# Performance work log

Hardware: AMD Instinct MI355X
Metric: run time of the kernel (lower is better)

## Reference

```python
import jax, jax.numpy as jnp
import numpy as np

N, D, C = 262144, 128, 64  # flattened tokens, feat_dim, num_classes (subjects)


def setup_inputs() -> dict:
    key = jax.random.key(0)
    k1, k2, k3 = jax.random.split(key, 3)
    feature = jax.random.normal(k1, (N, D), dtype=jnp.float32)
    label = jax.random.randint(k2, (N,), 0, C, dtype=jnp.int64)
    centers = jax.random.normal(k3, (C, D), dtype=jnp.float32)  # nn.Parameter torch.randn
    return {"feature": feature, "label": label, "centers": centers}


def reference(feature, label, centers):
    f = feature.reshape(-1, feature.shape[1])            # [N, D]
    lbl = label.reshape(-1)                              # [N]
    num_classes = centers.shape[0]

    # Pairwise squared distances ||f_i - c_j||^2, via expansion to avoid the
    # [N, C, D] broadcast intermediate the torch code materializes.
    f2 = jnp.sum(f * f, axis=1, keepdims=True)           # [N, 1]
    c2 = jnp.sum(centers * centers, axis=1)              # [C]
    distance_centers = f2 + c2[None, :] - 2.0 * (f @ centers.T)  # [N, C]

    centers_batch = centers[lbl]                         # [N, D] gather
    center_loss = jnp.mean((f - centers_batch) ** 2)     # MSELoss (mean reduction)

    diff = centers_batch - f                             # [N, D]
    # segment-reduce replacing the per-unique-label python loop
    sums = jax.ops.segment_sum(diff, lbl, num_segments=num_classes)      # [C, D]
    counts = jnp.bincount(lbl, length=num_classes)                        # [C]
    difference = sums / jnp.clip(counts, 1, None).astype(f.dtype)[:, None]

    return (center_loss, difference, distance_centers)
```

## Files before the change

kernel.cpp:

```cpp
#include <hip/hip_runtime.h>
#include <hip/hip_bf16.h>

#define N_TOK 262144
#define D_FEAT 128
#define C_CLS 64
#define TILE_M 128
#define DIST_BLOCKS 1024
#define BLOCK_T 256
#define TILES_PER_BLOCK 2
#define NSTEP (TILES_PER_BLOCK * 2)
#define SEG_ELEMS (C_CLS * D_FEAT)
#define SEG_BLOCKS 1024
#define SEG_ROWS_B (N_TOK / SEG_BLOCKS)
#define SEG_KSTEPS (SEG_ROWS_B / 32)

typedef __attribute__((ext_vector_type(8))) short bf16x8;
typedef __attribute__((ext_vector_type(4))) float f32x4;

__device__ __forceinline__ short f2bf(float x) {
    return (short)__bfloat16_as_ushort(__float2bfloat16(x));
}

__device__ __forceinline__ bf16x8 pack8(float4 a, float4 b) {
    bf16x8 t;
    t[0] = f2bf(a.x); t[1] = f2bf(a.y); t[2] = f2bf(a.z); t[3] = f2bf(a.w);
    t[4] = f2bf(b.x); t[5] = f2bf(b.y); t[6] = f2bf(b.z); t[7] = f2bf(b.w);
    return t;
}

__device__ __forceinline__ void gload_lds16(const float* g, float* l) {
    __builtin_amdgcn_global_load_lds(
        (const __attribute__((address_space(1))) void*)g,
        (__attribute__((address_space(3))) void*)l, 16, 0, 0);
}

__device__ __forceinline__ void stage_issue(const float* __restrict__ f,
                                            int rbase, float* buf, int lane) {
    const int rl = lane >> 5;
    const int dc = lane & 31;
    #pragma unroll
    for (int i = 0; i < 8; ++i) {
        const int r  = i * 2 + rl;
        const int sc = dc ^ (r & 7);
        gload_lds16(f + (size_t)(rbase + r) * D_FEAT + sc * 4,
                    buf + (i * 2) * D_FEAT);
    }
}

__global__ __launch_bounds__(BLOCK_T, 2) void dist_main(
    const float* __restrict__ f, const int* __restrict__ label,
    const float* __restrict__ centers, float* __restrict__ dist_out,
    float* __restrict__ ws_loss, float* __restrict__ ws_ploss, int mode)
{
    __shared__ float stage4[4][16][D_FEAT];
    __shared__ float c2s[C_CLS];
    __shared__ float f2t[TILE_M];
    __shared__ int   lblt[TILES_PER_BLOCK][TILE_M];
    __shared__ float wred[4];

    const int tid  = threadIdx.x;
    const int lane = tid & 63;
    const int w    = tid >> 6;
    const int qk   = lane >> 4;
    const int ln   = lane & 15;
    const int di   = blockIdx.x;

    float* buf = &stage4[w][0][0];

    stage_issue(f, di * TILE_M + w * 32, buf, lane);

    const int tt = lane >> 5;
    const int lr = lane & 31;
    const int lv = label[(di + tt * DIST_BLOCKS) * TILE_M + w * 32 + lr];

    if (tid < C_CLS) {
        float s = 0.f;
        const float* cp = centers + tid * D_FEAT;
        for (int k = 0; k < D_FEAT; k += 4) {
            float4 c4 = *(const float4*)(cp + k);
            s += c4.x*c4.x + c4.y*c4.y + c4.z*c4.z + c4.w*c4.w;
        }
        c2s[tid] = s;
    }

    bf16x8 bfr[4][4];
    #pragma unroll
    for (int ct = 0; ct < 4; ++ct) {
        const float* bp = centers + (ct * 16 + ln) * D_FEAT + qk * 8;
        #pragma unroll
        for (int ks = 0; ks < 4; ++ks) {
            float4 v0 = *(const float4*)(bp + ks * 32);
            float4 v1 = *(const float4*)(bp + ks * 32 + 4);
            bfr[ct][ks] = pack8(v0, v1);
        }
    }
    __syncthreads();
    lblt[tt][w * 32 + lr] = lv;

    float lossa = 0.f;

    for (int t = 0; t < NSTEP; ++t) {
        const int tl    = t >> 1;
        const int half  = t & 1;
        const int rbase = (di + tl * DIST_BLOCKS) * TILE_M + w * 32 + half * 16;

        if (t == 0) asm volatile("s_waitcnt vmcnt(0)" ::: "memory");
        else        asm volatile("s_waitcnt vmcnt(16)" ::: "memory");
        __builtin_amdgcn_sched_barrier(0);

        float4 v[8];
        #pragma unroll
        for (int ks = 0; ks < 4; ++ks) {
            const int g0 = ks * 8 + qk * 2;
            v[2*ks]   = *(const float4*)(buf + ln * D_FEAT + ((g0    ) ^ (ln & 7)) * 4);
            v[2*ks+1] = *(const float4*)(buf + ln * D_FEAT + ((g0 + 1) ^ (ln & 7)) * 4);
        }

        asm volatile("s_waitcnt lgkmcnt(0)" ::: "memory");
        __builtin_amdgcn_sched_barrier(0);
        if (t + 1 < NSTEP) {
            const int t1 = t + 1;
            stage_issue(f, (di + (t1 >> 1) * DIST_BLOCKS) * TILE_M
                           + w * 32 + (t1 & 1) * 16, buf, lane);
        }

        float s2 = 0.f;
        #pragma unroll
        for (int i = 0; i < 8; ++i)
            s2 += v[i].x*v[i].x + v[i].y*v[i].y + v[i].z*v[i].z + v[i].w*v[i].w;
        s2 += __shfl_xor(s2, 16);
        s2 += __shfl_xor(s2, 32);
        if (lane < 16) f2t[w * 32 + half * 16 + lane] = s2;

        bf16x8 afr[4];
        #pragma unroll
        for (int ks = 0; ks < 4; ++ks) afr[ks] = pack8(v[2*ks], v[2*ks+1]);

        const int mloc = w * 32 + half * 16 + qk * 4;
        #pragma unroll
        for (int ct = 0; ct < 4; ++ct) {
            f32x4 acc = {0.f, 0.f, 0.f, 0.f};
            #pragma unroll
            for (int ks = 0; ks < 4; ++ks)
                acc = __builtin_amdgcn_mfma_f32_16x16x32_bf16(
                    afr[ks], bfr[ct][ks], acc, 0, 0, 0);
            const int n    = ct * 16 + ln;
            const float cv = c2s[n];
            float* op = dist_out + (size_t)(rbase + qk * 4) * C_CLS + n;
            #pragma unroll
            for (int u = 0; u < 4; ++u) {
                const float dv = f2t[mloc + u] + cv - 2.f * acc[u];
                op[(size_t)u * C_CLS] = dv;
                if (lblt[tl][mloc + u] == n) lossa += dv;
            }
        }
    }

    #pragma unroll
    for (int off = 32; off; off >>= 1) lossa += __shfl_xor(lossa, off);
    if (mode == 1) {
        if (lane == 0) wred[w] = lossa;
        __syncthreads();
        if (tid == 0) ws_ploss[di] = wred[0] + wred[1] + wred[2] + wred[3];
    } else {
        if (lane == 0) unsafeAtomicAdd(ws_loss, lossa);
    }
}

__global__ __launch_bounds__(BLOCK_T, 4) void seg_main(
    const float* __restrict__ f, const int* __restrict__ label,
    float* __restrict__ ws_seg, unsigned* __restrict__ ws_cnt,
    float* __restrict__ ws_part, unsigned* __restrict__ ws_pcnt, int mode)
{
    __shared__ int      lblt[SEG_ROWS_B];
    __shared__ unsigned cnts[C_CLS];

    const int tid  = threadIdx.x;
    const int lane = tid & 63;
    const int w    = tid >> 6;
    const int qk   = lane >> 4;
    const int ln   = lane & 15;
    const int sb   = blockIdx.x;
    const int r0   = sb * SEG_ROWS_B;

    if (tid < C_CLS) cnts[tid] = 0u;
    __syncthreads();
    {
        const int lv = label[r0 + tid];
        lblt[tid] = lv;
        atomicAdd(&cnts[lv], 1u);
    }
    __syncthreads();

    const int cbase = w * 32;
    f32x4 acc[4][2];
    #pragma unroll
    for (int ct = 0; ct < 4; ++ct) {
        acc[ct][0] = (f32x4){0.f, 0.f, 0.f, 0.f};
        acc[ct][1] = (f32x4){0.f, 0.f, 0.f, 0.f};
    }

    for (int kk = 0; kk < SEG_KSTEPS; ++kk) {
        const int kr = kk * 32 + qk * 8;
        const float* bp = f + (size_t)(r0 + kr) * D_FEAT + cbase + ln;
        float b0[8], b1[8];
        #pragma unroll
        for (int j = 0; j < 8; ++j) {
            b0[j] = bp[(size_t)j * D_FEAT];
            b1[j] = bp[(size_t)j * D_FEAT + 16];
        }
        int lb[8];
        #pragma unroll
        for (int j = 0; j < 8; ++j) lb[j] = lblt[kr + j];
        bf16x8 bf0, bf1;
        #pragma unroll
        for (int j = 0; j < 8; ++j) { bf0[j] = f2bf(b0[j]); bf1[j] = f2bf(b1[j]); }
        #pragma unroll
        for (int ct = 0; ct < 4; ++ct) {
            const int cls = ct * 16 + ln;
            bf16x8 a;
            #pragma unroll
            for (int j = 0; j < 8; ++j)
                a[j] = (lb[j] == cls) ? (short)0x3F80 : (short)0;
            acc[ct][0] = __builtin_amdgcn_mfma_f32_16x16x32_bf16(a, bf0, acc[ct][0], 0, 0, 0);
            acc[ct][1] = __builtin_amdgcn_mfma_f32_16x16x32_bf16(a, bf1, acc[ct][1], 0, 0, 0);
        }
    }

    if (mode == 1) {
        float* dst = ws_part + (size_t)sb * SEG_ELEMS;
        #pragma unroll
        for (int ct = 0; ct < 4; ++ct)
            #pragma unroll
            for (int dt = 0; dt < 2; ++dt)
                #pragma unroll
                for (int u = 0; u < 4; ++u)
                    dst[(ct * 16 + qk * 4 + u) * D_FEAT + cbase + dt * 16 + ln] = acc[ct][dt][u];
        if (tid < C_CLS) ws_pcnt[sb * C_CLS + tid] = cnts[tid];
    } else {
        #pragma unroll
        for (int ct = 0; ct < 4; ++ct)
            for (int dt = 0; dt < 2; ++dt)
                for (int u = 0; u < 4; ++u)
                    unsafeAtomicAdd(&ws_seg[(ct * 16 + qk * 4 + u) * D_FEAT
                                            + cbase + dt * 16 + ln], acc[ct][dt][u]);
        if (tid < C_CLS) atomicAdd(&ws_cnt[tid], cnts[tid]);
    }
}

__global__ __launch_bounds__(256) void center_redfin(
    const float* __restrict__ ws_part, const unsigned* __restrict__ ws_pcnt,
    const float* __restrict__ ws_ploss, const float* __restrict__ centers,
    float* __restrict__ out)
{
    __shared__ float lred[4];
    __shared__ float cntf[2];
    const int tid = threadIdx.x;
    const int bid = blockIdx.x;
    const int i   = bid * 256 + tid;
    const int wv  = tid >> 6, wl = tid & 63;

    if (wv < 2) {
        const int c = bid * 2 + wv;
        unsigned cs = 0u;
        for (int b = wl; b < SEG_BLOCKS; b += 64) cs += ws_pcnt[b * C_CLS + c];
        #pragma unroll
        for (int off = 32; off; off >>= 1) cs += __shfl_xor(cs, off);
        if (wl == 0) cntf[wv] = (float)cs;
    }

    float s = 0.f;
    #pragma unroll 8
    for (int b = 0; b < SEG_BLOCKS; ++b)
        s += ws_part[(size_t)b * SEG_ELEMS + i];

    if (bid == 0) {
        float ls = ws_ploss[tid] + ws_ploss[tid + 256]
                 + ws_ploss[tid + 512] + ws_ploss[tid + 768];
        #pragma unroll
        for (int off = 32; off; off >>= 1) ls += __shfl_xor(ls, off);
        if (wl == 0) lred[wv] = ls;
    }
    __syncthreads();
    if (bid == 0 && tid == 0)
        out[0] = (lred[0] + lred[1] + lred[2] + lred[3])
               / ((float)N_TOK * (float)D_FEAT);

    const float cnt   = cntf[tid >> 7];
    const float denom = fmaxf(cnt, 1.f);
    out[1 + i] = (cnt * centers[i] - s) / denom;
}

__global__ void center_fin(const float* __restrict__ centers,
                           const float* __restrict__ ws_loss,
                           const unsigned* __restrict__ ws_cnt,
                           const float* __restrict__ ws_seg,
                           float* __restrict__ out)
{
    const int i = blockIdx.x * 256 + threadIdx.x;
    if (i == 0) out[0] = ws_loss[0] / ((float)N_TOK * (float)D_FEAT);
    if (i < SEG_ELEMS) {
        const int c = i >> 7;
        const unsigned cnt = ws_cnt[c];
        const float denom = (float)(cnt > 1u ? cnt : 1u);
        out[1 + i] = ((float)cnt * centers[i] - ws_seg[i]) / denom;
    }
}

extern "C" void kernel_launch(void* const* d_in, const int* in_sizes, int n_in,
                              void* d_out, int out_size, void* d_ws, size_t ws_size,
                              hipStream_t stream)
{
    const float* f       = (const float*)d_in[0];
    const int*   lbl     = (const int*)d_in[1];
    const float* centers = (const float*)d_in[2];
    float* out = (float*)d_out;

    float*    ws_loss  = (float*)d_ws;
    unsigned* ws_cnt   = (unsigned*)((char*)d_ws + 256);
    float*    ws_seg   = (float*)((char*)d_ws + 1024);
    char*     p        = (char*)d_ws + 1024 + SEG_ELEMS * sizeof(float);
    float*    ws_part  = (float*)p;
    unsigned* ws_pcnt  = (unsigned*)(p + (size_t)SEG_BLOCKS * SEG_ELEMS * sizeof(float));
    float*    ws_ploss = (float*)(p + (size_t)SEG_BLOCKS * SEG_ELEMS * sizeof(float)
                                     + (size_t)SEG_BLOCKS * C_CLS * sizeof(unsigned));

    const size_t need = 1024 + SEG_ELEMS * sizeof(float)
                      + (size_t)SEG_BLOCKS * SEG_ELEMS * sizeof(float)
                      + (size_t)SEG_BLOCKS * C_CLS * sizeof(unsigned)
                      + (size_t)DIST_BLOCKS * sizeof(float);

    float* dist_out = out + 1 + SEG_ELEMS;
    if (ws_size >= need) {
        dist_main<<<DIST_BLOCKS, BLOCK_T, 0, stream>>>(f, lbl, centers, dist_out,
                                                       ws_loss, ws_ploss, 1);
        seg_main<<<SEG_BLOCKS, BLOCK_T, 0, stream>>>(f, lbl, ws_seg, ws_cnt,
                                                     ws_part, ws_pcnt, 1);
        center_redfin<<<32, 256, 0, stream>>>(ws_part, ws_pcnt, ws_ploss,
                                              centers, out);
    } else {
        hipMemsetAsync(d_ws, 0, 1024 + SEG_ELEMS * sizeof(float), stream);
        dist_main<<<DIST_BLOCKS, BLOCK_T, 0, stream>>>(f, lbl, centers, dist_out,
                                                       ws_loss, ws_ploss, 0);
        seg_main<<<SEG_BLOCKS, BLOCK_T, 0, stream>>>(f, lbl, ws_seg, ws_cnt,
                                                     ws_part, ws_pcnt, 0);
        center_fin<<<32, 256, 0, stream>>>(centers, ws_loss, ws_cnt, ws_seg, out);
    }
}
```

Baseline: 294.5 us.

## Widen final reduction grid, transpose count partials, use nontemporal stores

The final reduction kernel goes from 32 to 128 blocks. Each block's four waves now split the 1024 partial slabs into quarters and combine them through shared memory, which gives more parallelism when reading the 32 MB partial buffer. Per-block counts are stored transposed so the count reduction reads contiguously. Nontemporal stores and loads are used for the distance output and the partial buffers to keep them out of cache. The cost is a little more shared-memory traffic and an extra barrier.

```diff
diff --git a/kernel.cpp b/kernel.cpp
--- a/kernel.cpp
+++ b/kernel.cpp
@@ -13,6 +13,7 @@
 #define SEG_BLOCKS 1024
 #define SEG_ROWS_B (N_TOK / SEG_BLOCKS)
 #define SEG_KSTEPS (SEG_ROWS_B / 32)
+#define REDF_BLOCKS 128
 
 typedef __attribute__((ext_vector_type(8))) short bf16x8;
 typedef __attribute__((ext_vector_type(4))) float f32x4;
@@ -150,7 +151,7 @@
             #pragma unroll
             for (int u = 0; u < 4; ++u) {
                 const float dv = f2t[mloc + u] + cv - 2.f * acc[u];
-                op[(size_t)u * C_CLS] = dv;
+                __builtin_nontemporal_store(dv, op + (size_t)u * C_CLS);
                 if (lblt[tl][mloc + u] == n) lossa += dv;
             }
         }
@@ -235,8 +236,10 @@
             for (int dt = 0; dt < 2; ++dt)
                 #pragma unroll
                 for (int u = 0; u < 4; ++u)
-                    dst[(ct * 16 + qk * 4 + u) * D_FEAT + cbase + dt * 16 + ln] = acc[ct][dt][u];
-        if (tid < C_CLS) ws_pcnt[sb * C_CLS + tid] = cnts[tid];
+                    __builtin_nontemporal_store(acc[ct][dt][u],
+                        &dst[(ct * 16 + qk * 4 + u) * D_FEAT + cbase + dt * 16 + ln]);
+        if (tid < C_CLS)
+            __builtin_nontemporal_store(cnts[tid], &ws_pcnt[tid * SEG_BLOCKS + sb]);
     } else {
         #pragma unroll
         for (int ct = 0; ct < 4; ++ct)
@@ -253,42 +256,51 @@
     const float* __restrict__ ws_ploss, const float* __restrict__ centers,
     float* __restrict__ out)
 {
-    __shared__ float lred[4];
-    __shared__ float cntf[2];
+    __shared__ float partial[4][64];
+    __shared__ float cntf;
+    __shared__ float lossv;
+
     const int tid = threadIdx.x;
     const int bid = blockIdx.x;
-    const int i   = bid * 256 + tid;
-    const int wv  = tid >> 6, wl = tid & 63;
-
-    if (wv < 2) {
-        const int c = bid * 2 + wv;
+    const int e   = tid & 63;
+    const int sc  = tid >> 6;
+    const int i   = bid * 64 + e;
+    const int c   = bid >> 1;
+
+    float s = 0.f;
+    const float* src = ws_part + (size_t)sc * 256 * SEG_ELEMS + i;
+    #pragma unroll 8
+    for (int k = 0; k < 256; ++k)
+        s += __builtin_nontemporal_load(src + (size_t)k * SEG_ELEMS);
+    partial[sc][e] = s;
+
+    if (sc == 1) {
         unsigned cs = 0u;
-        for (int b = wl; b < SEG_BLOCKS; b += 64) cs += ws_pcnt[b * C_CLS + c];
+        #pragma unroll 4
+        for (int b = e; b < SEG_BLOCKS; b += 64)
+            cs += __builtin_nontemporal_load(&ws_pcnt[c * SEG_BLOCKS + b]);
         #pragma unroll
         for (int off = 32; off; off >>= 1) cs += __shfl_xor(cs, off);
-        if (wl == 0) cntf[wv] = (float)cs;
-    }
-
-    float s = 0.f;
-    #pragma unroll 8
-    for (int b = 0; b < SEG_BLOCKS; ++b)
-        s += ws_part[(size_t)b * SEG_ELEMS + i];
-
-    if (bid == 0) {
-        float ls = ws_ploss[tid] + ws_ploss[tid + 256]
-                 + ws_ploss[tid + 512] + ws_ploss[tid + 768];
+        if (e == 0) cntf = (float)cs;
+    }
+    if (bid == 0 && sc == 2) {
+        float ls = 0.f;
+        #pragma unroll 4
+        for (int k = e; k < DIST_BLOCKS; k += 64)
+            ls += __builtin_nontemporal_load(&ws_ploss[k]);
         #pragma unroll
         for (int off = 32; off; off >>= 1) ls += __shfl_xor(ls, off);
-        if (wl == 0) lred[wv] = ls;
+        if (e == 0) lossv = ls;
     }
     __syncthreads();
+
     if (bid == 0 && tid == 0)
-        out[0] = (lred[0] + lred[1] + lred[2] + lred[3])
-               / ((float)N_TOK * (float)D_FEAT);
-
-    const float cnt   = cntf[tid >> 7];
-    const float denom = fmaxf(cnt, 1.f);
-    out[1 + i] = (cnt * centers[i] - s) / denom;
+        out[0] = lossv / ((float)N_TOK * (float)D_FEAT);
+    if (sc == 0) {
+        const float t   = partial[0][e] + partial[1][e] + partial[2][e] + partial[3][e];
+        const float cnt = cntf;
+        out[1 + i] = (cnt * centers[i] - t) / fmaxf(cnt, 1.f);
+    }
 }
 
 __global__ void center_fin(const float* __restrict__ centers,
@@ -336,8 +348,8 @@
                                                        ws_loss, ws_ploss, 1);
         seg_main<<<SEG_BLOCKS, BLOCK_T, 0, stream>>>(f, lbl, ws_seg, ws_cnt,
                                                      ws_part, ws_pcnt, 1);
-        center_redfin<<<32, 256, 0, stream>>>(ws_part, ws_pcnt, ws_ploss,
-                                              centers, out);
+        center_redfin<<<REDF_BLOCKS, 256, 0, stream>>>(ws_part, ws_pcnt, ws_ploss,
+                                                       centers, out);
     } else {
         hipMemsetAsync(d_ws, 0, 1024 + SEG_ELEMS * sizeof(float), stream);
         dist_main<<<DIST_BLOCKS, BLOCK_T, 0, stream>>>(f, lbl, centers, dist_out,
```

Result: slower. 302.7 us (+2.8%).
